# Optimization experiments

Hardware: AMD Instinct MI355X
Metric: run time of the kernel (lower is better)

Reference implementation:

```python
import jax, jax.numpy as jnp
import numpy as np

HEADS = 8
DIM_HEAD = 64
DIM = 512
INNER = HEADS * DIM_HEAD
NUM_FREQ_BANDS = 32
MAX_FREQ = 32
POS_DIM = 2 * (NUM_FREQ_BANDS * 2 + 1)  # 130
PHYS_SCALE = 51.5
ATTN_SCALE = DIM_HEAD ** -0.5


def fourier_encode(x, freqs):
    # x: [...], freqs: [F] -> [..., 2F+1]
    xs = x[..., None] * freqs * jnp.pi
    return jnp.concatenate([jnp.sin(xs), jnp.cos(xs), x[..., None]], axis=-1)


def polar_encoding(positions, freqs):
    # positions: [B, Ls, 2] -> [B, Ls, Ls, POS_DIM]; diff[b,i,j] = pos[b,j] - pos[b,i]
    diff = positions[:, None, :, :] - positions[:, :, None, :]
    dx, dy = diff[..., 0], diff[..., 1]
    r = jnp.sqrt(dx * dx + dy * dy + 1e-8)
    theta = jnp.arctan2(dy, dx)
    r_c = r / (PHYS_SCALE + r)
    th_n = theta / jnp.pi
    return jnp.concatenate([fourier_encode(r_c, freqs), fourier_encode(th_n, freqs)], axis=-1)


def setup_inputs() -> dict:
    key = jax.random.key(0)
    ks = jax.random.split(key, 8)
    B, L, Ls = 2, 272, 256
    x = jax.random.normal(ks[0], (B, L, DIM), dtype=jnp.float32)
    positions = jax.random.uniform(ks[1], (B, Ls, 2), dtype=jnp.float32) * 103.0
    Wq = jax.random.normal(ks[2], (DIM, INNER), dtype=jnp.float32) * 0.02
    Wk = jax.random.normal(ks[3], (DIM + POS_DIM, INNER), dtype=jnp.float32) * 0.02
    Wv = jax.random.normal(ks[4], (DIM + POS_DIM, INNER), dtype=jnp.float32) * 0.02
    Wo = jax.random.normal(ks[5], (INNER, DIM), dtype=jnp.float32) * 0.02
    bo = jnp.zeros((DIM,), dtype=jnp.float32)
    freqs = jnp.linspace(1.0, MAX_FREQ / 2.0, NUM_FREQ_BANDS, dtype=jnp.float32)
    return {"x": x, "positions": positions, "Wq": Wq, "Wk": Wk, "Wv": Wv,
            "Wo": Wo, "bo": bo, "freqs": freqs, "num_spatial": Ls}


def reference(x, positions, Wq, Wk, Wv, Wo, bo, freqs, num_spatial):
    B, L, D = x.shape
    Ls = num_spatial
    Lg = L - Ls
    x_sp = x[:, :Ls, :]
    x_gl = x[:, Ls:, :]

    # queries for all latents
    q = (x @ Wq).reshape(B, L, HEADS, DIM_HEAD).transpose(0, 2, 1, 3)  # [B,H,L,dh]
    q_sp, q_gl = q[:, :, :Ls, :], q[:, :, Ls:, :]

    # per-pair spatial K/V with polar PE
    pe = polar_encoding(positions, freqs)  # [B,Ls,Ls,POS_DIM]
    x_sp_exp = jnp.broadcast_to(x_sp[:, None, :, :], (B, Ls, Ls, D))
    x_sp_pe = jnp.concatenate([x_sp_exp, pe], axis=-1)  # [B,Ls,Ls,D+POS_DIM]
    k_sp = (x_sp_pe @ Wk).reshape(B, Ls, Ls, HEADS, DIM_HEAD).transpose(0, 3, 1, 2, 4)
    v_sp = (x_sp_pe @ Wv).reshape(B, Ls, Ls, HEADS, DIM_HEAD).transpose(0, 3, 1, 2, 4)

    # global K/V (zero PE)
    zpad_g = jnp.zeros((B, Lg, POS_DIM), dtype=x.dtype)
    x_gl_pe = jnp.concatenate([x_gl, zpad_g], axis=-1)
    k_gl = (x_gl_pe @ Wk).reshape(B, Lg, HEADS, DIM_HEAD).transpose(0, 2, 1, 3)
    v_gl = (x_gl_pe @ Wv).reshape(B, Lg, HEADS, DIM_HEAD).transpose(0, 2, 1, 3)

    # spatial queries attend to per-pair spatial K and global K
    attn_ss = jnp.einsum('bhid,bhijd->bhij', q_sp, k_sp) * ATTN_SCALE
    attn_sg = jnp.einsum('bhid,bhjd->bhij', q_sp, k_gl) * ATTN_SCALE
    attn_sp = jnp.concatenate([attn_ss, attn_sg], axis=-1)  # [B,H,Ls,L]

    # global queries attend to spatial (zero PE) and global keys
    zpad_s = jnp.zeros((B, Ls, POS_DIM), dtype=x.dtype)
    x_sp_zpe = jnp.concatenate([x_sp, zpad_s], axis=-1)
    k_sp_g = (x_sp_zpe @ Wk).reshape(B, Ls, HEADS, DIM_HEAD).transpose(0, 2, 1, 3)
    v_sp_g = (x_sp_zpe @ Wv).reshape(B, Ls, HEADS, DIM_HEAD).transpose(0, 2, 1, 3)
    attn_gs = jnp.einsum('bhid,bhjd->bhij', q_gl, k_sp_g) * ATTN_SCALE
    attn_gg = jnp.einsum('bhid,bhjd->bhij', q_gl, k_gl) * ATTN_SCALE
    attn_gl = jnp.concatenate([attn_gs, attn_gg], axis=-1)  # [B,H,Lg,L]

    attn = jax.nn.softmax(jnp.concatenate([attn_sp, attn_gl], axis=2), axis=-1)  # [B,H,L,L]

    a_ss = attn[:, :, :Ls, :Ls]
    a_sg = attn[:, :, :Ls, Ls:]
    a_gs = attn[:, :, Ls:, :Ls]
    a_gg = attn[:, :, Ls:, Ls:]

    out_sp = jnp.einsum('bhij,bhijd->bhid', a_ss, v_sp) + jnp.einsum('bhij,bhjd->bhid', a_sg, v_gl)
    out_gl = jnp.einsum('bhij,bhjd->bhid', a_gs, v_sp_g) + jnp.einsum('bhij,bhjd->bhid', a_gg, v_gl)
    out = jnp.concatenate([out_sp, out_gl], axis=2)  # [B,H,L,dh]
    out = out.transpose(0, 2, 1, 3).reshape(B, L, INNER)
    return out @ Wo + bo
```

## Files before the change

### kernel.cpp

```cpp
#include <hip/hip_runtime.h>
#include <math.h>

#define NHEADS 8
#define DHEAD 64
#define NDIM 512
#define NFREQ 32
#define POSD 130
#define NB 2
#define NL 272
#define NLS 256
#define NROWS (NB*NL)
#define ATTN_SCALE 0.125f
#define PHYS_SCALE 51.5f
#define PI_F 3.14159265358979323846f
#define USTR 168
#define PSTR 72
#define PART_STRIDE 264
#define SROWS 320
#define SCOLS 320
#define UCOLS 132

typedef short s16x8 __attribute__((ext_vector_type(8)));
typedef float f32x4 __attribute__((ext_vector_type(4)));

__device__ __forceinline__ short bfb(float x) {
  unsigned short u = __builtin_bit_cast(unsigned short, (__bf16)x);
  return (short)u;
}

__global__ __launch_bounds__(256) void qkv_gemm_k(
    const float* __restrict__ x,
    const float* __restrict__ Wq, const float* __restrict__ Wk,
    const float* __restrict__ Wv,
    float* __restrict__ qkv)
{
  __shared__ float As[16][68];
  __shared__ float Bs[16][64];
  const int t  = threadIdx.x;
  const int m0 = blockIdx.x * 64;
  const int ng = blockIdx.y * 64;
  const int region = ng >> 9;
  const int n0 = ng & 511;
  const float* W = (region == 0) ? Wq : (region == 1) ? Wk : Wv;
  float* out = qkv + (size_t)region * (NROWS * NDIM);

  const int tx = t & 15, ty = t >> 4;
  const int arow = t >> 2, akq = (t & 3) * 4;
  const int brow = t >> 4, bcol = (t & 15) * 4;

  float acc[4][4];
#pragma unroll
  for (int i = 0; i < 4; ++i)
#pragma unroll
    for (int j = 0; j < 4; ++j) acc[i][j] = 0.f;

  for (int k0 = 0; k0 < 512; k0 += 16) {
    float4 av = make_float4(0.f, 0.f, 0.f, 0.f);
    if (m0 + arow < NROWS)
      av = *(const float4*)&x[(size_t)(m0 + arow) * NDIM + k0 + akq];
    As[akq + 0][arow] = av.x; As[akq + 1][arow] = av.y;
    As[akq + 2][arow] = av.z; As[akq + 3][arow] = av.w;
    *(float4*)&Bs[brow][bcol] =
        *(const float4*)&W[(size_t)(k0 + brow) * NDIM + n0 + bcol];
    __syncthreads();
#pragma unroll
    for (int kk = 0; kk < 16; ++kk) {
      float4 a = *(const float4*)&As[kk][ty * 4];
      float4 b = *(const float4*)&Bs[kk][tx * 4];
      float aa[4] = {a.x, a.y, a.z, a.w};
      float bb[4] = {b.x, b.y, b.z, b.w};
#pragma unroll
      for (int i = 0; i < 4; ++i)
#pragma unroll
        for (int j = 0; j < 4; ++j) acc[i][j] = fmaf(aa[i], bb[j], acc[i][j]);
    }
    __syncthreads();
  }
#pragma unroll
  for (int i = 0; i < 4; ++i) {
    int row = m0 + ty * 4 + i;
    if (row < NROWS)
      *(float4*)&out[(size_t)row * NDIM + n0 + tx * 4] =
          make_float4(acc[i][0], acc[i][1], acc[i][2], acc[i][3]);
  }
}

__global__ __launch_bounds__(256) void su_gemm_k(
    const float* __restrict__ qb, const float* __restrict__ kb,
    const float* __restrict__ Wk,
    float* __restrict__ s_ws, short* __restrict__ u_ws)
{
  __shared__ float As[16][68];
  __shared__ float Bs[16][68];
  const int t = threadIdx.x;
  const int bx = blockIdx.x;
  const int b = bx / 5;
  const int m0 = (bx - b * 5) * 64;
  const int nt = blockIdx.y;
  const int h = blockIdx.z;
  const int n0 = nt * 64;

  const int tx = t & 15, ty = t >> 4;
  const int arow = t >> 2, akq = (t & 3) * 4;

  float acc[4][4];
#pragma unroll
  for (int i = 0; i < 4; ++i)
#pragma unroll
    for (int j = 0; j < 4; ++j) acc[i][j] = 0.f;

  for (int k0 = 0; k0 < 64; k0 += 16) {
    float4 av = make_float4(0.f, 0.f, 0.f, 0.f);
    {
      int i = m0 + arow;
      if (i < NL)
        av = *(const float4*)&qb[(size_t)(b * NL + i) * NDIM + h * DHEAD + k0 + akq];
    }
    As[akq + 0][arow] = av.x; As[akq + 1][arow] = av.y;
    As[akq + 2][arow] = av.z; As[akq + 3][arow] = av.w;
    float4 bv = make_float4(0.f, 0.f, 0.f, 0.f);
    if (nt < 5) {
      int j = n0 + arow;
      if (j < NL)
        bv = *(const float4*)&kb[(size_t)(b * NL + j) * NDIM + h * DHEAD + k0 + akq];
    } else {
      int f = n0 - 320 + arow;
      if (f < POSD)
        bv = *(const float4*)&Wk[(size_t)(512 + f) * NDIM + h * DHEAD + k0 + akq];
    }
    Bs[akq + 0][arow] = bv.x; Bs[akq + 1][arow] = bv.y;
    Bs[akq + 2][arow] = bv.z; Bs[akq + 3][arow] = bv.w;
    __syncthreads();
#pragma unroll
    for (int kk = 0; kk < 16; ++kk) {
      float4 a = *(const float4*)&As[kk][ty * 4];
      float4 b2 = *(const float4*)&Bs[kk][tx * 4];
      float aa[4] = {a.x, a.y, a.z, a.w};
      float bb[4] = {b2.x, b2.y, b2.z, b2.w};
#pragma unroll
      for (int i = 0; i < 4; ++i)
#pragma unroll
        for (int j = 0; j < 4; ++j) acc[i][j] = fmaf(aa[i], bb[j], acc[i][j]);
    }
    __syncthreads();
  }

  const size_t rowbase = (size_t)((h * NB + b) * SROWS + m0);
  if (nt < 5) {
#pragma unroll
    for (int ii = 0; ii < 4; ++ii) {
      size_t r = rowbase + ty * 4 + ii;
      *(float4*)&s_ws[r * SCOLS + n0 + tx * 4] =
          make_float4(acc[ii][0] * ATTN_SCALE, acc[ii][1] * ATTN_SCALE,
                      acc[ii][2] * ATTN_SCALE, acc[ii][3] * ATTN_SCALE);
    }
  } else {
#pragma unroll
    for (int ii = 0; ii < 4; ++ii) {
      size_t r = rowbase + ty * 4 + ii;
#pragma unroll
      for (int jj = 0; jj < 4; ++jj) {
        int f = n0 - 320 + tx * 4 + jj;
        if (f < POSD) u_ws[r * UCOLS + f] = bfb(acc[ii][jj]);
      }
    }
  }
}

__global__ __launch_bounds__(256) void out_gemm_k(
    const float* __restrict__ A, const float* __restrict__ Wo,
    const float* __restrict__ bo, float* __restrict__ out)
{
  __shared__ float As[16][68];
  __shared__ float Bs[16][64];
  const int t  = threadIdx.x;
  const int m0 = blockIdx.x * 64;
  const int n0 = blockIdx.y * 64;

  const int tx = t & 15, ty = t >> 4;
  const int arow = t >> 2, akq = (t & 3) * 4;
  const int brow = t >> 4, bcol = (t & 15) * 4;

  float acc[4][4];
#pragma unroll
  for (int i = 0; i < 4; ++i)
#pragma unroll
    for (int j = 0; j < 4; ++j) acc[i][j] = 0.f;

  for (int k0 = 0; k0 < 512; k0 += 16) {
    float4 av = make_float4(0.f, 0.f, 0.f, 0.f);
    if (m0 + arow < NROWS)
      av = *(const float4*)&A[(size_t)(m0 + arow) * NDIM + k0 + akq];
    As[akq + 0][arow] = av.x; As[akq + 1][arow] = av.y;
    As[akq + 2][arow] = av.z; As[akq + 3][arow] = av.w;
    *(float4*)&Bs[brow][bcol] =
        *(const float4*)&Wo[(size_t)(k0 + brow) * NDIM + n0 + bcol];
    __syncthreads();
#pragma unroll
    for (int kk = 0; kk < 16; ++kk) {
      float4 a = *(const float4*)&As[kk][ty * 4];
      float4 b = *(const float4*)&Bs[kk][tx * 4];
      float aa[4] = {a.x, a.y, a.z, a.w};
      float bb[4] = {b.x, b.y, b.z, b.w};
#pragma unroll
      for (int i = 0; i < 4; ++i)
#pragma unroll
        for (int j = 0; j < 4; ++j) acc[i][j] = fmaf(aa[i], bb[j], acc[i][j]);
    }
    __syncthreads();
  }
  float4 bv = *(const float4*)&bo[n0 + tx * 4];
  float bb[4] = {bv.x, bv.y, bv.z, bv.w};
#pragma unroll
  for (int i = 0; i < 4; ++i) {
    int row = m0 + ty * 4 + i;
    if (row < NROWS)
      *(float4*)&out[(size_t)row * NDIM + n0 + tx * 4] =
          make_float4(acc[i][0] + bb[0], acc[i][1] + bb[1],
                      acc[i][2] + bb[2], acc[i][3] + bb[3]);
  }
}

__global__ __launch_bounds__(256) void attn_pe_k(
    const float* __restrict__ s_ws, const short* __restrict__ u_ws,
    const float* __restrict__ vb, const float* __restrict__ pos,
    const float* __restrict__ Wv, const float* __restrict__ freqs,
    float* __restrict__ part)
{
  __shared__ short u_s[16 * USTR];
  __shared__ short p_bf[16 * PSTR];
  __shared__ float p_s[4][64];
  __shared__ float s_l[4][64];
  __shared__ float s_pe[4][64];
  __shared__ float w_s[4][160];
  __shared__ float rc_s[128], th_s[128];
  __shared__ float frp_s[NFREQ];
  __shared__ float m_s[4], l_s[4], fac_s[4];

  const int row = blockIdx.x;
  const int hg  = blockIdx.y;
  const int ks  = blockIdx.z;
  const int b = row / NL;
  const int i = row - b * NL;
  const bool spatial = (i < NLS);
  const int t = threadIdx.x;
  const int lane = t & 63;
  const int wv = t >> 6;
  const int g = lane >> 4;
  const int lr = lane & 15;
  const int hbase = hg * 4;
  const int h4 = t >> 6;
  const int dd = t & 63;

  for (int idx = t; idx < 16 * USTR / 2; idx += 256) ((int*)u_s)[idx] = 0;
  for (int idx = t; idx < 16 * PSTR / 2; idx += 256) ((int*)p_bf)[idx] = 0;
  if (t < NFREQ) frp_s[t] = freqs[t] * PI_F;
  if (t < 4) { m_s[t] = -1e30f; l_s[t] = 0.f; }
  __syncthreads();

  float px = 0.f, py = 0.f;
  if (spatial) {
    float2 pv = *(const float2*)&pos[(size_t)(b * NLS + i) * 2];
    px = pv.x; py = pv.y;
  }
  if (spatial && t < 128) {
    int key = ks * 128 + t;
    float2 kp = *(const float2*)&pos[(size_t)(b * NLS + key) * 2];
    float dx = kp.x - px, dy = kp.y - py;
    float r = sqrtf(dx * dx + dy * dy + 1e-8f);
    rc_s[t] = r / (PHYS_SCALE + r);
    th_s[t] = atan2f(dy, dx) * (1.0f / PI_F);
  }
  if (spatial) {
    for (int idx = t; idx < 4 * POSD; idx += 256) {
      int hh = idx / POSD, f = idx - hh * POSD;
      int slot = (f < 64) ? f : (f == 64) ? 128 : (f == 129) ? 129 : f - 1;
      u_s[hh * USTR + slot] =
          u_ws[((size_t)((hbase + hh) * NB + b) * SROWS + i) * UCOLS + f];
    }
  }
  __syncthreads();

  float oA = 0.f, oB = 0.f;
  f32x4 wacc[3];
#pragma unroll
  for (int q = 0; q < 3; ++q) wacc[q] = (f32x4){0.f, 0.f, 0.f, 0.f};

  for (int ti = 0; ti < 2; ++ti) {
    const int kloc = ks * 128 + ti * 64;
    const int koff = ti * 64;

    s_l[h4][dd] =
        s_ws[((size_t)((hbase + h4) * NB + b) * SROWS + i) * SCOLS + kloc + dd];
    if (spatial) {
      const int keyloc = koff + wv * 16 + lr;
      const float rc = rc_s[keyloc], th = th_s[keyloc];
      const float* frp = &frp_s[g * 8];
      s16x8 a0, a1, a2, a3, a4;
#pragma unroll
      for (int j = 0; j < 8; ++j) {
        float s1, c1, s2, c2;
        __sincosf(rc * frp[j], &s1, &c1);
        __sincosf(th * frp[j], &s2, &c2);
        a0[j] = bfb(s1); a1[j] = bfb(c1); a2[j] = bfb(s2); a3[j] = bfb(c2);
        a4[j] = 0;
      }
      if (g == 0) { a4[0] = bfb(rc); a4[1] = bfb(th); }
      const short* ur = &u_s[lr * USTR + g * 8];
      f32x4 acc = (f32x4){0.f, 0.f, 0.f, 0.f};
      acc = __builtin_amdgcn_mfma_f32_16x16x32_bf16(a0, *(const s16x8*)(ur), acc, 0, 0, 0);
      acc = __builtin_amdgcn_mfma_f32_16x16x32_bf16(a1, *(const s16x8*)(ur + 32), acc, 0, 0, 0);
      acc = __builtin_amdgcn_mfma_f32_16x16x32_bf16(a2, *(const s16x8*)(ur + 64), acc, 0, 0, 0);
      acc = __builtin_amdgcn_mfma_f32_16x16x32_bf16(a3, *(const s16x8*)(ur + 96), acc, 0, 0, 0);
      acc = __builtin_amdgcn_mfma_f32_16x16x32_bf16(a4, *(const s16x8*)(ur + 128), acc, 0, 0, 0);
      if (lr < 4) {
#pragma unroll
        for (int r = 0; r < 4; ++r)
          s_pe[lr][wv * 16 + g * 4 + r] = acc[r] * ATTN_SCALE;
      }
    }
    __syncthreads();

    {
      float v = s_l[h4][dd];
      if (spatial) v += s_pe[h4][dd];
      float mx = v;
#pragma unroll
      for (int off = 32; off > 0; off >>= 1)
        mx = fmaxf(mx, __shfl_xor(mx, off, 64));
      float m_old = m_s[h4];
      float m_new = fmaxf(m_old, mx);
      float p = __expf(v - m_new);
      p_s[h4][dd] = p;
      p_bf[h4 * PSTR + dd] = bfb(p);
      float sum = p;
#pragma unroll
      for (int off = 32; off > 0; off >>= 1)
        sum += __shfl_xor(sum, off, 64);
      if (lane == 0) {
        float fac = __expf(m_old - m_new);
        m_s[h4] = m_new;
        l_s[h4] = l_s[h4] * fac + sum;
        fac_s[h4] = fac;
      }
    }
    __syncthreads();

    {
      float fac = fac_s[h4];
      oA *= fac; oB *= fac;
      const float* vbase = &vb[(size_t)(b * NL + kloc) * NDIM + (hbase + h4) * DHEAD + dd];
      const float* pp = p_s[h4];
#pragma unroll 8
      for (int j = 0; j < 64; j += 2) {
        oA = fmaf(pp[j], vbase[(size_t)j * NDIM], oA);
        oB = fmaf(pp[j + 1], vbase[(size_t)(j + 1) * NDIM], oB);
      }
    }
    if (spatial) {
      const float facw = fac_s[lr & 3];
#pragma unroll
      for (int q = 0; q < 3; ++q) {
        const int mc = wv + q * 4;
        if (mc < 10) {
#pragma unroll
          for (int r = 0; r < 4; ++r) wacc[q][r] *= facw;
          const int s = mc * 16 + lr;
          const float Fp = frp_s[s & 31];
          const bool useTh = (s >= 64 && s < 128) || (s == 129);
          const bool useCos = (s & 32) != 0;
#pragma unroll
          for (int kc = 0; kc < 2; ++kc) {
            s16x8 a;
#pragma unroll
            for (int jj = 0; jj < 8; ++jj) {
              const int j = koff + kc * 32 + g * 8 + jj;
              float x = useTh ? th_s[j] : rc_s[j];
              float v;
              if (s < 128) {
                float sn, cs;
                __sincosf(x * Fp, &sn, &cs);
                v = useCos ? cs : sn;
              } else {
                v = (s < 130) ? x : 0.f;
              }
              a[jj] = bfb(v);
            }
            const s16x8 pb = *(const s16x8*)&p_bf[lr * PSTR + kc * 32 + g * 8];
            wacc[q] = __builtin_amdgcn_mfma_f32_16x16x32_bf16(a, pb, wacc[q], 0, 0, 0);
          }
        }
      }
    }
    __syncthreads();
  }

  if (ks == 1) {
    if (t < 64) {
      const int hh = t >> 4, j = t & 15;
      s_l[hh][j] =
          s_ws[((size_t)((hbase + hh) * NB + b) * SROWS + i) * SCOLS + 256 + j];
    }
    __syncthreads();
    {
      float v = (dd < 16) ? s_l[h4][dd] : -1e30f;
      float mx = v;
#pragma unroll
      for (int off = 32; off > 0; off >>= 1)
        mx = fmaxf(mx, __shfl_xor(mx, off, 64));
      float m_old = m_s[h4];
      float m_new = fmaxf(m_old, mx);
      float p = (dd < 16) ? __expf(v - m_new) : 0.f;
      if (dd < 16) p_s[h4][dd] = p;
      float sum = p;
#pragma unroll
      for (int off = 32; off > 0; off >>= 1)
        sum += __shfl_xor(sum, off, 64);
      if (lane == 0) {
        float fac = __expf(m_old - m_new);
        m_s[h4] = m_new;
        l_s[h4] = l_s[h4] * fac + sum;
        fac_s[h4] = fac;
      }
    }
    __syncthreads();
    {
      float fac = fac_s[h4];
      oA *= fac; oB *= fac;
      const float* vbase = &vb[(size_t)(b * NL + 256) * NDIM + (hbase + h4) * DHEAD + dd];
      const float* pp = p_s[h4];
#pragma unroll 4
      for (int j = 0; j < 16; j += 2) {
        oA = fmaf(pp[j], vbase[(size_t)j * NDIM], oA);
        oB = fmaf(pp[j + 1], vbase[(size_t)(j + 1) * NDIM], oB);
      }
    }
    if (spatial) {
      const float facw = fac_s[lr & 3];
#pragma unroll
      for (int q = 0; q < 3; ++q)
#pragma unroll
        for (int r = 0; r < 4; ++r) wacc[q][r] *= facw;
    }
  }

  __syncthreads();
  if (spatial && lr < 4) {
#pragma unroll
    for (int q = 0; q < 3; ++q) {
      const int mc = wv + q * 4;
      if (mc < 10) {
#pragma unroll
        for (int r = 0; r < 4; ++r)
          w_s[lr][mc * 16 + g * 4 + r] = wacc[q][r];
      }
    }
  }
  __syncthreads();

  float o = oA + oB;
  if (spatial) {
    const float* wsr = w_s[h4];
    const float* wvb = &Wv[(size_t)512 * NDIM + (hbase + h4) * DHEAD + dd];
    float e0 = 0.f, e1 = 0.f;
#pragma unroll 4
    for (int sf = 0; sf < 64; sf += 2) {
      e0 = fmaf(wsr[sf], wvb[(size_t)sf * NDIM], e0);
      e1 = fmaf(wsr[sf + 1], wvb[(size_t)(sf + 1) * NDIM], e1);
    }
#pragma unroll 4
    for (int sf = 64; sf < 128; sf += 2) {
      e0 = fmaf(wsr[sf], wvb[(size_t)(sf + 1) * NDIM], e0);
      e1 = fmaf(wsr[sf + 1], wvb[(size_t)(sf + 2) * NDIM], e1);
    }
    e0 = fmaf(wsr[128], wvb[(size_t)64 * NDIM], e0);
    e1 = fmaf(wsr[129], wvb[(size_t)129 * NDIM], e1);
    o += e0 + e1;
  }
  float* prow = part + ((size_t)(ks * NROWS + row) * 2 + hg) * PART_STRIDE;
  prow[t] = o;
  if (t < 4) { prow[256 + t] = m_s[t]; prow[260 + t] = l_s[t]; }
}

__global__ __launch_bounds__(256) void combine_k(
    const float* __restrict__ part, float* __restrict__ ao)
{
  const int row = blockIdx.x;
  const int hg = blockIdx.y;
  const int t = threadIdx.x;
  const int h4 = t >> 6;

  const float* p0 = part + ((size_t)(0 * NROWS + row) * 2 + hg) * PART_STRIDE;
  const float* p1 = part + ((size_t)(1 * NROWS + row) * 2 + hg) * PART_STRIDE;
  float m0 = p0[256 + h4], m1 = p1[256 + h4];
  float M = fmaxf(m0, m1);
  float f0 = __expf(m0 - M), f1 = __expf(m1 - M);
  float L = p0[260 + h4] * f0 + p1[260 + h4] * f1;
  ao[(size_t)row * NDIM + hg * 256 + t] = (p0[t] * f0 + p1[t] * f1) / L;
}

extern "C" void kernel_launch(void* const* d_in, const int* in_sizes, int n_in,
                              void* d_out, int out_size, void* d_ws, size_t ws_size,
                              hipStream_t stream)
{
  (void)in_sizes; (void)n_in; (void)out_size; (void)ws_size;
  const float* x     = (const float*)d_in[0];
  const float* pos   = (const float*)d_in[1];
  const float* Wq    = (const float*)d_in[2];
  const float* Wk    = (const float*)d_in[3];
  const float* Wv    = (const float*)d_in[4];
  const float* Wo    = (const float*)d_in[5];
  const float* bo    = (const float*)d_in[6];
  const float* freqs = (const float*)d_in[7];

  float* ws = (float*)d_ws;
  float* qkv  = ws;
  float* qb   = qkv;
  float* kb   = qkv + (size_t)NROWS * NDIM;
  float* vb   = qkv + (size_t)2 * NROWS * NDIM;
  float* ao   = qkv + (size_t)3 * NROWS * NDIM;
  float* part = ao  + (size_t)NROWS * NDIM;
  float* s_ws = part + (size_t)2 * NROWS * 2 * PART_STRIDE;
  short* u_ws = (short*)(s_ws + (size_t)NHEADS * NB * SROWS * SCOLS);

  qkv_gemm_k<<<dim3(9, 24), 256, 0, stream>>>(x, Wq, Wk, Wv, qkv);
  su_gemm_k<<<dim3(10, 8, 8), 256, 0, stream>>>(qb, kb, Wk, s_ws, u_ws);
  attn_pe_k<<<dim3(NROWS, 2, 2), 256, 0, stream>>>(s_ws, u_ws, vb, pos, Wv, freqs, part);
  combine_k<<<dim3(NROWS, 2), 256, 0, stream>>>(part, ao);
  out_gemm_k<<<dim3(9, 8), 256, 0, stream>>>(ao, Wo, bo, (float*)d_out);
}
```

Measured before the change: 124.3 us.

## Cache PE tile in LDS and generate Fourier terms by angle-addition recurrence

The Fourier positional features are now computed once per key tile, written into a shared-memory tile, and read back when accumulating the value-side PE weights, where they used to be recomputed with sincos. Within each group of 8 bands, sin/cos come from the angle-addition recurrence rather than a separate sincos per band. This relies on the frequencies being evenly spaced (linspace). It adds about 21KB of LDS per block, which can lower occupancy, and the recurrence adds small rounding error before the bf16 cast.

```diff
diff --git a/kernel.cpp b/kernel.cpp
--- a/kernel.cpp
+++ b/kernel.cpp
@@ -15,6 +15,7 @@
 #define PI_F 3.14159265358979323846f
 #define USTR 168
 #define PSTR 72
+#define PESTR 168
 #define PART_STRIDE 264
 #define SROWS 320
 #define SCOLS 320
@@ -229,6 +230,7 @@
 {
   __shared__ short u_s[16 * USTR];
   __shared__ short p_bf[16 * PSTR];
+  __shared__ short pe_lds[64 * PESTR];
   __shared__ float p_s[4][64];
   __shared__ float s_l[4][64];
   __shared__ float s_pe[4][64];
@@ -293,19 +295,37 @@
     s_l[h4][dd] =
         s_ws[((size_t)((hbase + h4) * NB + b) * SROWS + i) * SCOLS + kloc + dd];
     if (spatial) {
-      const int keyloc = koff + wv * 16 + lr;
-      const float rc = rc_s[keyloc], th = th_s[keyloc];
-      const float* frp = &frp_s[g * 8];
+      const int krow = wv * 16 + lr;
+      const float rc = rc_s[koff + krow], th = th_s[koff + krow];
+      const float f0 = frp_s[g * 8];
+      const float dphi = frp_s[1] - frp_s[0];
+      float sr, cr, st_, ct_;
+      __sincosf(rc * f0, &sr, &cr);
+      __sincosf(th * f0, &st_, &ct_);
+      float srd, crd, std_, ctd;
+      __sincosf(rc * dphi, &srd, &crd);
+      __sincosf(th * dphi, &std_, &ctd);
       s16x8 a0, a1, a2, a3, a4;
 #pragma unroll
       for (int j = 0; j < 8; ++j) {
-        float s1, c1, s2, c2;
-        __sincosf(rc * frp[j], &s1, &c1);
-        __sincosf(th * frp[j], &s2, &c2);
-        a0[j] = bfb(s1); a1[j] = bfb(c1); a2[j] = bfb(s2); a3[j] = bfb(c2);
+        a0[j] = bfb(sr); a1[j] = bfb(cr); a2[j] = bfb(st_); a3[j] = bfb(ct_);
         a4[j] = 0;
+        float nsr = fmaf(sr, crd, cr * srd);
+        float ncr = fmaf(cr, crd, -sr * srd);
+        sr = nsr; cr = ncr;
+        float nst = fmaf(st_, ctd, ct_ * std_);
+        float nct = fmaf(ct_, ctd, -st_ * std_);
+        st_ = nst; ct_ = nct;
       }
       if (g == 0) { a4[0] = bfb(rc); a4[1] = bfb(th); }
+      {
+        short* pr = &pe_lds[krow * PESTR];
+        *(s16x8*)&pr[g * 8]       = a0;
+        *(s16x8*)&pr[32 + g * 8]  = a1;
+        *(s16x8*)&pr[64 + g * 8]  = a2;
+        *(s16x8*)&pr[96 + g * 8]  = a3;
+        *(s16x8*)&pr[128 + g * 8] = a4;
+      }
       const short* ur = &u_s[lr * USTR + g * 8];
       f32x4 acc = (f32x4){0.f, 0.f, 0.f, 0.f};
       acc = __builtin_amdgcn_mfma_f32_16x16x32_bf16(a0, *(const s16x8*)(ur), acc, 0, 0, 0);
@@ -366,25 +386,13 @@
 #pragma unroll
           for (int r = 0; r < 4; ++r) wacc[q][r] *= facw;
           const int s = mc * 16 + lr;
-          const float Fp = frp_s[s & 31];
-          const bool useTh = (s >= 64 && s < 128) || (s == 129);
-          const bool useCos = (s & 32) != 0;
 #pragma unroll
           for (int kc = 0; kc < 2; ++kc) {
             s16x8 a;
 #pragma unroll
             for (int jj = 0; jj < 8; ++jj) {
-              const int j = koff + kc * 32 + g * 8 + jj;
-              float x = useTh ? th_s[j] : rc_s[j];
-              float v;
-              if (s < 128) {
-                float sn, cs;
-                __sincosf(x * Fp, &sn, &cs);
-                v = useCos ? cs : sn;
-              } else {
-                v = (s < 130) ? x : 0.f;
-              }
-              a[jj] = bfb(v);
+              const int j = kc * 32 + g * 8 + jj;
+              a[jj] = pe_lds[j * PESTR + s];
             }
             const s16x8 pb = *(const s16x8*)&p_bf[lr * PSTR + kc * 32 + g * 8];
             wacc[q] = __builtin_amdgcn_mfma_f32_16x16x32_bf16(a, pb, wacc[q], 0, 0, 0);
```

Result: faster. 119.8 us (-3.6%).
